# Kernel optimization log

Hardware: AMD Instinct MI355X
Metric: run time of the kernel (lower is better)

## Reference

```python
import jax, jax.numpy as jnp
import numpy as np

HOP_NUM = 3
N_NODES = 40000
N_EDGES = 640000
IN_DIM = 128
N_ALPHAS = HOP_NUM * (HOP_NUM + 1) // 2  # triangular layerRegular params


def setup_inputs() -> dict:
    key = jax.random.key(0)
    k_h, k_d, k_a, k_s, k_t = jax.random.split(key, 5)
    h = jax.random.normal(k_h, (N_NODES, IN_DIM), dtype=jnp.float32)
    d = jax.random.uniform(k_d, (N_NODES,), dtype=jnp.float32)  # degree normalization per node
    alphas = jax.random.uniform(k_a, (N_ALPHAS,), dtype=jnp.float32)
    src = jax.random.randint(k_s, (N_EDGES,), 0, N_NODES, dtype=jnp.int32)
    dst = jax.random.randint(k_t, (N_EDGES,), 0, N_NODES, dtype=jnp.int32)
    return {"h": h, "d": d, "alphas": alphas, "src": src, "dst": dst}


def reference(h, d, alphas, src, dst):
    n = h.shape[0]
    # edge_applying: e = 1 * d[dst] * d[src]  (symmetric-normalized edge weight)
    e = d[dst] * d[src]                      # [E]
    outs = [h]
    k = 0
    for i in range(HOP_NUM):
        feat = h
        for q in range(i + 1):
            # update_all(u_mul_e('h','e'), sum): agg[v] = sum_{(u,v)} feat[u] * e
            msg = feat[src] * e[:, None]     # [E, D]
            agg = jax.ops.segment_sum(msg, dst, num_segments=n)  # [N, D]
            a = alphas[k]; k += 1
            feat = agg * a + (1.0 - a) * feat
            # feature_drop with p=0.0 (eval) is identity
        outs.append(feat)
    return jnp.concatenate(outs, axis=1)       # [N, (HOP_NUM+1)*D]
```

## Files before the change

### kernel.cpp

```cpp
#include <hip/hip_runtime.h>


#define NN  40000
#define NE  640000
#define CAP 64
#define NCH 4
#define CWU 16

typedef unsigned int uint;
typedef unsigned short ushort;
typedef uint  u32x4 __attribute__((ext_vector_type(4)));
typedef float f32x2 __attribute__((ext_vector_type(2)));

__device__ inline ushort f2h(float f) {
    _Float16 h = (_Float16)f;
    return *(ushort*)&h;
}
__device__ inline float h2f(ushort u) {
    _Float16 h = *(_Float16*)&u;
    return (float)h;
}
__device__ inline ushort f2bf(float f) {
    uint x = __float_as_uint(f);
    x += 0x7fffu + ((x >> 16) & 1u);
    return (ushort)(x >> 16);
}
__device__ inline uint pack_bf2(float x, float y) {
    return ((uint)f2bf(y) << 16) | (uint)f2bf(x);
}
__device__ inline float bflo(uint u) { return __uint_as_float(u << 16); }
__device__ inline float bfhi(uint u) { return __uint_as_float(u & 0xffff0000u); }

__global__ __launch_bounds__(256) void build_k(
    const int* __restrict__ src, const int* __restrict__ dst,
    const float* __restrict__ deg,
    int* __restrict__ counts, uint* __restrict__ buck) {
    int e = blockIdx.x * 256 + threadIdx.x;
    int s = __builtin_nontemporal_load(src + e);
    int v = __builtin_nontemporal_load(dst + e);
    int slot = atomicAdd(&counts[v], 1);
    if (slot < CAP) {
        float w = deg[s] * deg[v];
        buck[v * CAP + slot] = ((uint)f2h(w) << 16) | (uint)s;
    }
}

__global__ __launch_bounds__(256) void cvt_k(
    const float* __restrict__ h, uint* __restrict__ tab) {
    int b   = blockIdx.x;
    int c   = (b & 7) >> 1;
    int wi  = (b >> 3) * 2 + (b & 1);
    int tgl = wi * 256 + threadIdx.x;
    int v = tgl >> 4, t = tgl & 15;
    f32x2 f = __builtin_nontemporal_load(
        (const f32x2*)(h + (size_t)v * 128 + c * 32 + t * 2));
    tab[(size_t)c * NN * CWU + tgl] = pack_bf2(f.x, f.y);
}

__device__ inline void gather_c(
    const uint* __restrict__ tabc,
    const int* __restrict__ counts, const uint* __restrict__ buck,
    int v, int t, float* a0, float* a1) {
    int cnt = counts[v];
    if (cnt > CAP) cnt = CAP;
    const uint* brow = buck + (size_t)v * CAP;
    float x0 = 0.f, x1 = 0.f;
    for (int j = 0; j < cnt; j += 4) {
        u32x4 bw = *(const u32x4*)(brow + j);
#pragma unroll
        for (int k = 0; k < 4; ++k) {
            bool ok = (j + k) < cnt;
            uint u  = bw[k];
            float w = ok ? h2f((ushort)(u >> 16)) : 0.f;
            int   s = ok ? (int)(u & 0xffffu) : 0;
            uint  f = tabc[(size_t)s * CWU + t];
            x0 = fmaf(w, bflo(f), x0);
            x1 = fmaf(w, bfhi(f), x1);
        }
    }
    *a0 = x0; *a1 = x1;
}

__global__ __launch_bounds__(256) void agg_k(
    const uint* __restrict__ tin, const int* __restrict__ counts,
    const uint* __restrict__ buck, uint* __restrict__ tout) {
    int b  = blockIdx.x;
    int c  = (b & 7) >> 1;
    int wi = (b >> 3) * 2 + (b & 1);
    int lane = threadIdx.x & 63, wave = threadIdx.x >> 6;
    int n = lane >> 4, t = lane & 15;
    int v = wi * 16 + wave * 4 + n;
    float a0, a1;
    gather_c(tin + (size_t)c * NN * CWU, counts, buck, v, t, &a0, &a1);
    tout[(size_t)c * NN * CWU + (size_t)v * CWU + t] = pack_bf2(a0, a1);
}

__global__ __launch_bounds__(256) void agg3_k(
    const uint* __restrict__ p2t, const uint* __restrict__ p1t,
    const float* __restrict__ h, const int* __restrict__ counts,
    const uint* __restrict__ buck, const float* __restrict__ alphas,
    float* __restrict__ out) {
    int b  = blockIdx.x;
    int c  = (b & 7) >> 1;
    int wi = (b >> 3) * 2 + (b & 1);
    int lane = threadIdx.x & 63, wave = threadIdx.x >> 6;
    int n = lane >> 4, t = lane & 15;
    int v = wi * 16 + wave * 4 + n;
    float p30, p31;
    gather_c(p2t + (size_t)c * NN * CWU, counts, buck, v, t, &p30, &p31);

    float a0 = alphas[0], a1 = alphas[1], a2 = alphas[2];
    float a3 = alphas[3], a4 = alphas[4], a5 = alphas[5];
    float c1p = a0, c1h = 1.f - a0;
    float c2pp = a2 * a1;
    float c2p  = a2 * (1.f - a1) + (1.f - a2) * a1;
    float c2h  = (1.f - a2) * (1.f - a1);
    float s2pp = a4 * a3;
    float s2p  = a4 * (1.f - a3) + (1.f - a4) * a3;
    float s2h  = (1.f - a4) * (1.f - a3);
    float c3ppp = a5 * s2pp;
    float c3pp  = a5 * s2p + (1.f - a5) * s2pp;
    float c3p   = a5 * s2h + (1.f - a5) * s2p;
    float c3h   = (1.f - a5) * s2h;

    size_t idx = (size_t)c * NN * CWU + (size_t)v * CWU + t;
    uint u1 = p1t[idx], u2 = p2t[idx];
    float q10 = bflo(u1), q11 = bfhi(u1);
    float q20 = bflo(u2), q21 = bfhi(u2);
    f32x2 hf = __builtin_nontemporal_load(
        (const f32x2*)(h + (size_t)v * 128 + c * 32 + t * 2));

    f32x2 r1, r2, r3;
    r1.x = c1p * q10 + c1h * hf.x;
    r1.y = c1p * q11 + c1h * hf.y;
    r2.x = c2pp * q20 + c2p * q10 + c2h * hf.x;
    r2.y = c2pp * q21 + c2p * q11 + c2h * hf.y;
    r3.x = c3ppp * p30 + c3pp * q20 + c3p * q10 + c3h * hf.x;
    r3.y = c3ppp * p31 + c3pp * q21 + c3p * q11 + c3h * hf.y;

    float* o = out + (size_t)v * 512 + c * 32 + t * 2;
    __builtin_nontemporal_store(hf, (f32x2*)(o));
    __builtin_nontemporal_store(r1, (f32x2*)(o + 128));
    __builtin_nontemporal_store(r2, (f32x2*)(o + 256));
    __builtin_nontemporal_store(r3, (f32x2*)(o + 384));
}

extern "C" void kernel_launch(void* const* d_in, const int* in_sizes, int n_in,
                              void* d_out, int out_size, void* d_ws, size_t ws_size,
                              hipStream_t stream) {
    const float* h      = (const float*)d_in[0];
    const float* deg    = (const float*)d_in[1];
    const float* alphas = (const float*)d_in[2];
    const int*   src    = (const int*)d_in[3];
    const int*   dst    = (const int*)d_in[4];
    float* out = (float*)d_out;

    char* ws = (char*)d_ws;
    int*  counts = (int*)(ws + 0);
    uint* buck   = (uint*)(ws + 160000);
    uint* hb     = (uint*)(ws + 10400000);
    uint* p1b    = (uint*)(ws + 20640000);
    uint* p2b    = (uint*)(ws + 30880000);

    hipMemsetAsync(counts, 0, NN * sizeof(int), stream);
    build_k<<<NE / 256, 256, 0, stream>>>(src, dst, deg, counts, buck);
    cvt_k<<<NN * NCH * CWU / 256, 256, 0, stream>>>(h, hb);

    agg_k<<<NN * NCH / 16, 256, 0, stream>>>(hb,  counts, buck, p1b);
    agg_k<<<NN * NCH / 16, 256, 0, stream>>>(p1b, counts, buck, p2b);
    agg3_k<<<NN * NCH / 16, 256, 0, stream>>>(p2b, p1b, h, counts, buck,
                                              alphas, out);
}
```

Baseline: 247.7 us.

## Replace fixed-capacity edge buckets with padded CSR built by count, scan, fill

Swaps the fixed 64-slot per-node bucket array for a compact CSR layout whose rows are padded to multiples of four. Building it now takes a count kernel, a single-block prefix scan and a fill kernel, plus a memset that zeroes the padding slots. The goal is to shrink the edge structure from about 10 MB to about 3 MB and remove the capacity cap, so the three gather passes stream less edge data. The cost is two extra kernel launches, a serial single-block scan, and a second atomic pass over all edges.

```diff
diff --git a/kernel.cpp b/kernel.cpp
--- a/kernel.cpp
+++ b/kernel.cpp
@@ -3,13 +3,11 @@
 
 #define NN  40000
 #define NE  640000
-#define CAP 64
 #define NCH 4
 #define CWU 16
 
 typedef unsigned int uint;
 typedef unsigned short ushort;
-typedef uint  u32x4 __attribute__((ext_vector_type(4)));
 typedef float f32x2 __attribute__((ext_vector_type(2)));
 
 __device__ inline ushort f2h(float f) {
@@ -31,18 +29,55 @@
 __device__ inline float bflo(uint u) { return __uint_as_float(u << 16); }
 __device__ inline float bfhi(uint u) { return __uint_as_float(u & 0xffff0000u); }
 
-__global__ __launch_bounds__(256) void build_k(
+__global__ __launch_bounds__(256) void count_k(
+    const int* __restrict__ dst, int* __restrict__ counts) {
+    int e = blockIdx.x * 256 + threadIdx.x;
+    int v = __builtin_nontemporal_load(dst + e);
+    atomicAdd(&counts[v], 1);
+}
+
+__global__ __launch_bounds__(1024) void scan_k(
+    const int* __restrict__ counts, int* __restrict__ offs,
+    int* __restrict__ cursor) {
+    __shared__ int part[1024];
+    int tid = threadIdx.x;
+    int base = tid * 40;
+    int s = 0;
+    for (int i = 0; i < 40; ++i) {
+        int idx = base + i;
+        if (idx < NN) s += (counts[idx] + 3) & ~3;
+    }
+    part[tid] = s;
+    __syncthreads();
+    for (int d = 1; d < 1024; d <<= 1) {
+        int v = part[tid];
+        int a = (tid >= d) ? part[tid - d] : 0;
+        __syncthreads();
+        part[tid] = v + a;
+        __syncthreads();
+    }
+    int run = (tid > 0) ? part[tid - 1] : 0;
+    for (int i = 0; i < 40; ++i) {
+        int idx = base + i;
+        if (idx < NN) {
+            offs[idx] = run;
+            cursor[idx] = run;
+            run += (counts[idx] + 3) & ~3;
+        }
+    }
+    if (tid == 1023) offs[NN] = part[1023];
+}
+
+__global__ __launch_bounds__(256) void fill_k(
     const int* __restrict__ src, const int* __restrict__ dst,
     const float* __restrict__ deg,
-    int* __restrict__ counts, uint* __restrict__ buck) {
+    int* __restrict__ cursor, uint* __restrict__ csr) {
     int e = blockIdx.x * 256 + threadIdx.x;
     int s = __builtin_nontemporal_load(src + e);
     int v = __builtin_nontemporal_load(dst + e);
-    int slot = atomicAdd(&counts[v], 1);
-    if (slot < CAP) {
-        float w = deg[s] * deg[v];
-        buck[v * CAP + slot] = ((uint)f2h(w) << 16) | (uint)s;
-    }
+    float w = deg[s] * deg[v];
+    int slot = atomicAdd(&cursor[v], 1);
+    csr[slot] = ((uint)f2h(w) << 16) | (uint)s;
 }
 
 __global__ __launch_bounds__(256) void cvt_k(
@@ -58,32 +93,34 @@
 }
 
 __device__ inline void gather_c(
-    const uint* __restrict__ tabc,
-    const int* __restrict__ counts, const uint* __restrict__ buck,
-    int v, int t, float* a0, float* a1) {
-    int cnt = counts[v];
-    if (cnt > CAP) cnt = CAP;
-    const uint* brow = buck + (size_t)v * CAP;
+    const uint* __restrict__ tabc, const int* __restrict__ offs,
+    const uint* __restrict__ csr, int v, int t, float* a0, float* a1) {
+    int o0 = offs[v], o1 = offs[v + 1];
     float x0 = 0.f, x1 = 0.f;
-    for (int j = 0; j < cnt; j += 4) {
-        u32x4 bw = *(const u32x4*)(brow + j);
-#pragma unroll
-        for (int k = 0; k < 4; ++k) {
-            bool ok = (j + k) < cnt;
-            uint u  = bw[k];
-            float w = ok ? h2f((ushort)(u >> 16)) : 0.f;
-            int   s = ok ? (int)(u & 0xffffu) : 0;
-            uint  f = tabc[(size_t)s * CWU + t];
-            x0 = fmaf(w, bflo(f), x0);
-            x1 = fmaf(w, bfhi(f), x1);
-        }
+    for (int j = o0; j < o1; j += 4) {
+        uint u0 = csr[j + 0];
+        uint u1 = csr[j + 1];
+        uint u2 = csr[j + 2];
+        uint u3 = csr[j + 3];
+        uint f0 = tabc[(size_t)(u0 & 0xffffu) * CWU + t];
+        uint f1 = tabc[(size_t)(u1 & 0xffffu) * CWU + t];
+        uint f2 = tabc[(size_t)(u2 & 0xffffu) * CWU + t];
+        uint f3 = tabc[(size_t)(u3 & 0xffffu) * CWU + t];
+        float w0 = h2f((ushort)(u0 >> 16));
+        float w1 = h2f((ushort)(u1 >> 16));
+        float w2 = h2f((ushort)(u2 >> 16));
+        float w3 = h2f((ushort)(u3 >> 16));
+        x0 = fmaf(w0, bflo(f0), x0); x1 = fmaf(w0, bfhi(f0), x1);
+        x0 = fmaf(w1, bflo(f1), x0); x1 = fmaf(w1, bfhi(f1), x1);
+        x0 = fmaf(w2, bflo(f2), x0); x1 = fmaf(w2, bfhi(f2), x1);
+        x0 = fmaf(w3, bflo(f3), x0); x1 = fmaf(w3, bfhi(f3), x1);
     }
     *a0 = x0; *a1 = x1;
 }
 
 __global__ __launch_bounds__(256) void agg_k(
-    const uint* __restrict__ tin, const int* __restrict__ counts,
-    const uint* __restrict__ buck, uint* __restrict__ tout) {
+    const uint* __restrict__ tin, const int* __restrict__ offs,
+    const uint* __restrict__ csr, uint* __restrict__ tout) {
     int b  = blockIdx.x;
     int c  = (b & 7) >> 1;
     int wi = (b >> 3) * 2 + (b & 1);
@@ -91,14 +128,14 @@
     int n = lane >> 4, t = lane & 15;
     int v = wi * 16 + wave * 4 + n;
     float a0, a1;
-    gather_c(tin + (size_t)c * NN * CWU, counts, buck, v, t, &a0, &a1);
+    gather_c(tin + (size_t)c * NN * CWU, offs, csr, v, t, &a0, &a1);
     tout[(size_t)c * NN * CWU + (size_t)v * CWU + t] = pack_bf2(a0, a1);
 }
 
 __global__ __launch_bounds__(256) void agg3_k(
     const uint* __restrict__ p2t, const uint* __restrict__ p1t,
-    const float* __restrict__ h, const int* __restrict__ counts,
-    const uint* __restrict__ buck, const float* __restrict__ alphas,
+    const float* __restrict__ h, const int* __restrict__ offs,
+    const uint* __restrict__ csr, const float* __restrict__ alphas,
     float* __restrict__ out) {
     int b  = blockIdx.x;
     int c  = (b & 7) >> 1;
@@ -107,7 +144,7 @@
     int n = lane >> 4, t = lane & 15;
     int v = wi * 16 + wave * 4 + n;
     float p30, p31;
-    gather_c(p2t + (size_t)c * NN * CWU, counts, buck, v, t, &p30, &p31);
+    gather_c(p2t + (size_t)c * NN * CWU, offs, csr, v, t, &p30, &p31);
 
     float a0 = alphas[0], a1 = alphas[1], a2 = alphas[2];
     float a3 = alphas[3], a4 = alphas[4], a5 = alphas[5];
@@ -157,17 +194,22 @@
 
     char* ws = (char*)d_ws;
     int*  counts = (int*)(ws + 0);
-    uint* buck   = (uint*)(ws + 160000);
-    uint* hb     = (uint*)(ws + 10400000);
-    uint* p1b    = (uint*)(ws + 20640000);
-    uint* p2b    = (uint*)(ws + 30880000);
+    int*  offs   = (int*)(ws + 160000);
+    int*  cursor = (int*)(ws + 320016);
+    uint* csr    = (uint*)(ws + 480064);
+    uint* hb     = (uint*)(ws + 3680256);
+    uint* p1b    = (uint*)(ws + 13920256);
+    uint* p2b    = (uint*)(ws + 24160256);
 
     hipMemsetAsync(counts, 0, NN * sizeof(int), stream);
-    build_k<<<NE / 256, 256, 0, stream>>>(src, dst, deg, counts, buck);
+    hipMemsetAsync(csr, 0, 3200000, stream);
+    count_k<<<NE / 256, 256, 0, stream>>>(dst, counts);
+    scan_k<<<1, 1024, 0, stream>>>(counts, offs, cursor);
+    fill_k<<<NE / 256, 256, 0, stream>>>(src, dst, deg, cursor, csr);
     cvt_k<<<NN * NCH * CWU / 256, 256, 0, stream>>>(h, hb);
 
-    agg_k<<<NN * NCH / 16, 256, 0, stream>>>(hb,  counts, buck, p1b);
-    agg_k<<<NN * NCH / 16, 256, 0, stream>>>(p1b, counts, buck, p2b);
-    agg3_k<<<NN * NCH / 16, 256, 0, stream>>>(p2b, p1b, h, counts, buck,
+    agg_k<<<NN * NCH / 16, 256, 0, stream>>>(hb,  offs, csr, p1b);
+    agg_k<<<NN * NCH / 16, 256, 0, stream>>>(p1b, offs, csr, p2b);
+    agg3_k<<<NN * NCH / 16, 256, 0, stream>>>(p2b, p1b, h, offs, csr,
                                               alphas, out);
 }
```

After: 360.5 us. +45.5%, slower.
